# Kernel tuning notes

Hardware: AMD Instinct MI355X
Metric: run time of the kernel (lower is better)

## Reference

```python
import jax, jax.numpy as jnp
import numpy as np

D = 256      # embedding_dim
DI = 512     # inner dim = proj_factor * D
H = 4        # num heads
DH = DI // H # head dim
L = 4        # num blocks
K = 4        # causal conv kernel size

def _ln(x, g, b):
    mu = jnp.mean(x, -1, keepdims=True)
    v = jnp.var(x, -1, keepdims=True)
    return (x - mu) * jax.lax.rsqrt(v + 1e-5) * g + b

def _causal_conv(x, w, b):
    # x [B,S,DI], w [K,DI] depthwise causal conv
    S = x.shape[1]
    xp = jnp.pad(x, ((0, 0), (K - 1, 0), (0, 0)))
    out = b
    for j in range(K):
        out = out + xp[:, j:j + S, :] * w[j]
    return out

def _mlstm(q, k, v, ip, fp):
    # parallel stabilized mLSTM. q,k,v [B,S,H,DH]; ip,fp [B,S,H]
    q = q.transpose(0, 2, 1, 3)
    k = k.transpose(0, 2, 1, 3)
    v = v.transpose(0, 2, 1, 3)
    ip = ip.transpose(0, 2, 1)  # [B,H,S]
    fp = fp.transpose(0, 2, 1)
    lf = jax.nn.log_sigmoid(fp)                      # log forget gates
    Fc = jnp.cumsum(lf, axis=-1)
    Fc = jnp.concatenate([jnp.zeros_like(Fc[..., :1]), Fc], axis=-1)  # [B,H,S+1]
    logfg = Fc[..., 1:, None] - Fc[..., None, 1:]    # [B,H,S,S]: sum of log f over (s,t]
    S_len = q.shape[2]
    tri = jnp.tril(jnp.ones((S_len, S_len), dtype=bool))
    logD = jnp.where(tri, logfg + ip[..., None, :], jnp.float32(-1e30))
    m = jnp.max(logD, axis=-1, keepdims=True)        # stabilizer
    Dm = jnp.exp(logD - m)
    qk = jnp.einsum('bhtd,bhsd->bhts', q, k) * (DH ** -0.5)
    C = qk * Dm
    norm = jnp.maximum(jnp.abs(jnp.sum(C, axis=-1, keepdims=True)), jnp.exp(-m))
    h = jnp.einsum('bhts,bhsd->bhtd', C / (norm + 1e-6), v)
    return h.transpose(0, 2, 1, 3)

def _forward(x, time_features, Wp, bp, ln_g, ln_b, Wup, bup, conv_w, conv_b,
             Wq, Wk, Wv, Wif, bif, gn_g, gn_b, skip, Wdown, bdown,
             lnf_g, lnf_b, Wf, bf):
    B, S = x.shape
    xi = jnp.concatenate([x[..., None], time_features], axis=-1)  # [B,S,5]
    h = xi @ Wp + bp                                              # [B,S,D]
    for l in range(L):
        res = h
        hn = _ln(h, ln_g[l], ln_b[l])
        up = hn @ Wup[l] + bup[l]                 # [B,S,2*DI]
        xm, z = up[..., :DI], up[..., DI:]
        xc = jax.nn.silu(_causal_conv(xm, conv_w[l], conv_b[l]))
        q = (xc @ Wq[l]).reshape(B, S, H, DH)
        k = (xc @ Wk[l]).reshape(B, S, H, DH)
        v = (xm @ Wv[l]).reshape(B, S, H, DH)
        gi = jnp.concatenate([q.reshape(B, S, DI), k.reshape(B, S, DI), v.reshape(B, S, DI)], axis=-1)
        gates = gi @ Wif[l] + bif[l]              # [B,S,2H]
        ht = _mlstm(q, k, v, gates[..., :H], gates[..., H:])  # [B,S,H,DH]
        ht = _ln(ht, gn_g[l].reshape(H, DH), gn_b[l].reshape(H, DH)).reshape(B, S, DI)
        ht = ht + skip[l] * xc
        ht = ht * jax.nn.silu(z)
        h = res + ht @ Wdown[l] + bdown[l]
    h = _ln(h, lnf_g, lnf_b)
    return h[:, -1, :] @ Wf + bf                  # [B,1]

def setup_inputs():
    key = jax.random.key(0)
    ks = jax.random.split(key, 16)
    B, S = 8, 1024
    sd = jnp.float32(0.02)
    return {
        'x': jax.random.normal(ks[0], (B, S), jnp.float32),
        'time_features': jax.random.normal(ks[1], (B, S, 4), jnp.float32),
        'Wp': jax.random.normal(ks[2], (5, D)) * sd, 'bp': jnp.zeros((D,)),
        'ln_g': jnp.ones((L, D)), 'ln_b': jnp.zeros((L, D)),
        'Wup': jax.random.normal(ks[3], (L, D, 2 * DI)) * sd, 'bup': jnp.zeros((L, 2 * DI)),
        'conv_w': jax.random.normal(ks[4], (L, K, DI)) * sd, 'conv_b': jnp.zeros((L, DI)),
        'Wq': jax.random.normal(ks[5], (L, DI, DI)) * sd,
        'Wk': jax.random.normal(ks[6], (L, DI, DI)) * sd,
        'Wv': jax.random.normal(ks[7], (L, DI, DI)) * sd,
        'Wif': jax.random.normal(ks[8], (L, 3 * DI, 2 * H)) * sd, 'bif': jnp.zeros((L, 2 * H)),
        'gn_g': jnp.ones((L, DI)), 'gn_b': jnp.zeros((L, DI)),
        'skip': jnp.ones((L, DI)),
        'Wdown': jax.random.normal(ks[9], (L, DI, D)) * sd, 'bdown': jnp.zeros((L, D)),
        'lnf_g': jnp.ones((D,)), 'lnf_b': jnp.zeros((D,)),
        'Wf': jax.random.normal(ks[10], (D, 1)) * sd, 'bf': jnp.zeros((1,)),
    }

def reference(x, time_features, Wp, bp, ln_g, ln_b, Wup, bup, conv_w, conv_b,
              Wq, Wk, Wv, Wif, bif, gn_g, gn_b, skip, Wdown, bdown,
              lnf_g, lnf_b, Wf, bf):
    return _forward(x, time_features, Wp, bp, ln_g, ln_b, Wup, bup, conv_w, conv_b,
                    Wq, Wk, Wv, Wif, bif, gn_g, gn_b, skip, Wdown, bdown,
                    lnf_g, lnf_b, Wf, bf)
```

## Files before the change

### kernel.cpp

```cpp
#include <hip/hip_runtime.h>
#include <hip/hip_bf16.h>
#include <math.h>

#define S 1024
#define NLAYER 4

typedef __bf16 bf16x8 __attribute__((ext_vector_type(8)));
typedef float floatx4 __attribute__((ext_vector_type(4)));

__device__ __forceinline__ float wave_sum(float v) {
  #pragma unroll
  for (int off = 32; off > 0; off >>= 1) v += __shfl_xor(v, off, 64);
  return v;
}

__device__ __forceinline__ void wtrans_body(
    int bid, const float* Wup, const float* Wq, const float* Wk, const float* Wv,
    const float* Wdown, __bf16* WupT, __bf16* WqkT, __bf16* WvT, __bf16* WdownT) {
  __shared__ float T[32][33];
  int layer = bid / 1152, rr = bid % 1152;
  const float* src; __bf16* dst; int K, N, tile;
  if (rr < 256)       { src = Wup   + layer * 262144; dst = WupT  + layer * 262144;          K = 256; N = 1024; tile = rr; }
  else if (rr < 512)  { src = Wq    + layer * 262144; dst = WqkT  + layer * 524288;          K = 512; N = 512;  tile = rr - 256; }
  else if (rr < 768)  { src = Wk    + layer * 262144; dst = WqkT  + layer * 524288 + 262144; K = 512; N = 512;  tile = rr - 512; }
  else if (rr < 1024) { src = Wv    + layer * 262144; dst = WvT   + layer * 262144;          K = 512; N = 512;  tile = rr - 768; }
  else                { src = Wdown + layer * 131072; dst = WdownT + layer * 131072;         K = 512; N = 256;  tile = rr - 1024; }
  int ntn = N >> 5;
  int tk = tile / ntn, tn = tile % ntn;
  int tid = threadIdx.x;
  int r = tid >> 3, c4 = (tid & 7) * 4;
  float4 v = *(const float4*)(src + (size_t)(tk * 32 + r) * N + tn * 32 + c4);
  T[c4 + 0][r] = v.x; T[c4 + 1][r] = v.y; T[c4 + 2][r] = v.z; T[c4 + 3][r] = v.w;
  __syncthreads();
  __bf16 o[4];
  #pragma unroll
  for (int j = 0; j < 4; ++j) o[j] = (__bf16)T[r][c4 + j];
  *(uint2*)(dst + (size_t)(tn * 32 + r) * K + tk * 32 + c4) = *(uint2*)o;
}

__device__ __forceinline__ void wgprep_body(
    int bid, const float* Wq, const float* Wk, const float* Wv,
    const float* Wif, float* wg) {
  int l = bid >> 8;
  int rem = bid & 255;
  int sel = rem >> 7;
  int kg = rem & 127;
  int tid = threadIdx.x;
  int wv = tid >> 6, lane = tid & 63;
  int k = kg * 4 + wv;
  const float* wif = Wif + (size_t)l * 1536 * 8;
  float part[8] = {0, 0, 0, 0, 0, 0, 0, 0};
  if (sel == 0) {
    const float* qr = Wq + (size_t)l * 262144 + (size_t)k * 512;
    const float* kr = Wk + (size_t)l * 262144 + (size_t)k * 512;
    #pragma unroll
    for (int i = 0; i < 8; ++i) {
      int n = lane + i * 64;
      float qv = qr[n], kv = kr[n];
      const float* wq8 = wif + (size_t)n * 8;
      const float* wk8 = wif + (size_t)(512 + n) * 8;
      #pragma unroll
      for (int j = 0; j < 8; ++j) part[j] += qv * wq8[j] + kv * wk8[j];
    }
  } else {
    const float* vr = Wv + (size_t)l * 262144 + (size_t)k * 512;
    #pragma unroll
    for (int i = 0; i < 8; ++i) {
      int n = lane + i * 64;
      float vv = vr[n];
      const float* wv8 = wif + (size_t)(1024 + n) * 8;
      #pragma unroll
      for (int j = 0; j < 8; ++j) part[j] += vv * wv8[j];
    }
  }
  #pragma unroll
  for (int j = 0; j < 8; ++j) part[j] = wave_sum(part[j]);
  if (lane < 8) wg[(size_t)l * 8192 + sel * 4096 + (size_t)k * 8 + lane] = part[lane];
}

__device__ __forceinline__ void embed_body(
    int row, const float* x, const float* tf, const float* Wp, const float* bp,
    const float* g, const float* b, float* h, __bf16* hn) {
  int n = threadIdx.x;
  float xv = x[row];
  const float* t4 = tf + (size_t)row * 4;
  float acc = bp[n] + xv * Wp[n];
  acc += t4[0] * Wp[256 + n];
  acc += t4[1] * Wp[512 + n];
  acc += t4[2] * Wp[768 + n];
  acc += t4[3] * Wp[1024 + n];
  h[(size_t)row * 256 + n] = acc;
  __shared__ float red[4];
  int wid = n >> 6, lane = n & 63;
  float s = wave_sum(acc);
  if (lane == 0) red[wid] = s;
  __syncthreads();
  float mu = (red[0] + red[1] + red[2] + red[3]) * (1.f / 256.f);
  __syncthreads();
  float d = acc - mu;
  float s2 = wave_sum(d * d);
  if (lane == 0) red[wid] = s2;
  __syncthreads();
  float var = (red[0] + red[1] + red[2] + red[3]) * (1.f / 256.f);
  float rs = rsqrtf(var + 1e-5f);
  hn[(size_t)row * 256 + n] = (__bf16)(d * rs * g[n] + b[n]);
}

__global__ __launch_bounds__(256) void prep_kernel(
    const float* __restrict__ x, const float* __restrict__ tf,
    const float* __restrict__ Wp, const float* __restrict__ bp,
    const float* __restrict__ ln_g, const float* __restrict__ ln_b,
    const float* __restrict__ Wup, const float* __restrict__ Wq,
    const float* __restrict__ Wk, const float* __restrict__ Wv,
    const float* __restrict__ Wdown, const float* __restrict__ Wif,
    __bf16* __restrict__ WupT, __bf16* __restrict__ WqkT,
    __bf16* __restrict__ WvT, __bf16* __restrict__ WdownT,
    float* __restrict__ wg, float* __restrict__ h, __bf16* __restrict__ hn) {
  int bid = blockIdx.x;
  if (bid < 4608) {
    wtrans_body(bid, Wup, Wq, Wk, Wv, Wdown, WupT, WqkT, WvT, WdownT);
  } else if (bid < 4608 + 1024) {
    wgprep_body(bid - 4608, Wq, Wk, Wv, Wif, wg);
  } else {
    embed_body(bid - 5632, x, tf, Wp, bp, ln_g, ln_b, h, hn);
  }
}

__global__ __launch_bounds__(256) void ln256_kernel(
    const float* __restrict__ x, const float* __restrict__ g,
    const float* __restrict__ b, __bf16* __restrict__ y) {
  int row = blockIdx.x, tid = threadIdx.x;
  __shared__ float red[4];
  float v = x[(size_t)row * 256 + tid];
  float s = wave_sum(v);
  int wid = tid >> 6, lane = tid & 63;
  if (lane == 0) red[wid] = s;
  __syncthreads();
  float mu = (red[0] + red[1] + red[2] + red[3]) * (1.f / 256.f);
  __syncthreads();
  float d = v - mu;
  float s2 = wave_sum(d * d);
  if (lane == 0) red[wid] = s2;
  __syncthreads();
  float var = (red[0] + red[1] + red[2] + red[3]) * (1.f / 256.f);
  float rs = rsqrtf(var + 1e-5f);
  y[(size_t)row * 256 + tid] = (__bf16)(d * rs * g[tid] + b[tid]);
}

template <int TM, int MODE, int ACC>
__device__ __forceinline__ void hgemm_body(
    char* smem_raw,
    const __bf16* __restrict__ A, int lda,
    const __bf16* __restrict__ BT, int Kdim,
    const float* __restrict__ bias,
    void* __restrict__ Cout, int ldc, int bxi, int byi) {
  auto As = (__bf16(*)[40])smem_raw;
  auto Bs = (__bf16(*)[40])(smem_raw + (size_t)TM * 80);
  int tid = threadIdx.x;
  int bm = bxi * TM, bn = byi * 128;
  int wid = tid >> 6, lane = tid & 63;
  int wr = wid >> 1, wc = wid & 1;
  int lg = lane >> 4, li = lane & 15;
  constexpr int MI = TM / 32;
  constexpr int WROW = TM / 2;
  floatx4 acc[MI][4];
  #pragma unroll
  for (int i = 0; i < MI; ++i)
    #pragma unroll
    for (int j = 0; j < 4; ++j) acc[i][j] = (floatx4)(0.f);

  int arow = tid >> 2, aseg = tid & 3;
  bf16x8 pa0, pa1, pb0, pb1;
  auto pre = [&](int k0) {
    pa0 = *(const bf16x8*)(A + (size_t)(bm + arow) * lda + k0 + aseg * 8);
    if constexpr (TM == 128)
      pa1 = *(const bf16x8*)(A + (size_t)(bm + arow + 64) * lda + k0 + aseg * 8);
    pb0 = *(const bf16x8*)(BT + (size_t)(bn + arow) * Kdim + k0 + aseg * 8);
    pb1 = *(const bf16x8*)(BT + (size_t)(bn + arow + 64) * Kdim + k0 + aseg * 8);
  };
  pre(0);
  for (int k0 = 0; k0 < Kdim; k0 += 32) {
    __syncthreads();
    if constexpr (TM == 128) {
      *(bf16x8*)&As[arow][aseg * 8] = pa0;
      *(bf16x8*)&As[arow + 64][aseg * 8] = pa1;
    } else {
      *(bf16x8*)&As[arow][aseg * 8] = pa0;
    }
    *(bf16x8*)&Bs[arow][aseg * 8] = pb0;
    *(bf16x8*)&Bs[arow + 64][aseg * 8] = pb1;
    __syncthreads();
    if (k0 + 32 < Kdim) pre(k0 + 32);
    bf16x8 af[MI], bfr[4];
    #pragma unroll
    for (int mi = 0; mi < MI; ++mi)
      af[mi] = *(const bf16x8*)&As[wr * WROW + mi * 16 + li][lg * 8];
    #pragma unroll
    for (int ni = 0; ni < 4; ++ni)
      bfr[ni] = *(const bf16x8*)&Bs[wc * 64 + ni * 16 + li][lg * 8];
    #pragma unroll
    for (int mi = 0; mi < MI; ++mi)
      #pragma unroll
      for (int ni = 0; ni < 4; ++ni)
        acc[mi][ni] = __builtin_amdgcn_mfma_f32_16x16x32_bf16(af[mi], bfr[ni], acc[mi][ni], 0, 0, 0);
  }
  if constexpr (MODE == 1) {
    __bf16* eb = (__bf16*)smem_raw;
    const int PITCH = 136;
    __bf16* C = (__bf16*)Cout;
    #pragma unroll
    for (int mi = 0; mi < MI; ++mi) {
      __syncthreads();
      #pragma unroll
      for (int ni = 0; ni < 4; ++ni) {
        int col = wc * 64 + ni * 16 + li;
        float bz = bias ? bias[bn + col] : 0.f;
        #pragma unroll
        for (int r = 0; r < 4; ++r) {
          int lr = wr * 16 + lg * 4 + r;
          eb[lr * PITCH + col] = (__bf16)(acc[mi][ni][r] + bz);
        }
      }
      __syncthreads();
      #pragma unroll
      for (int i = 0; i < 2; ++i) {
        int lr = (tid >> 4) + i * 16;
        int c8 = (tid & 15) * 8;
        bf16x8 v = *(const bf16x8*)&eb[lr * PITCH + c8];
        int row_g = bm + (lr >> 4) * 64 + mi * 16 + (lr & 15);
        *(bf16x8*)(C + (size_t)row_g * ldc + bn + c8) = v;
      }
    }
  } else {
    #pragma unroll
    for (int mi = 0; mi < MI; ++mi) {
      int row = bm + wr * WROW + mi * 16 + lg * 4;
      #pragma unroll
      for (int ni = 0; ni < 4; ++ni) {
        int col = bn + wc * 64 + ni * 16 + li;
        if constexpr (MODE == 2) {
          __bf16 o4[4];
          #pragma unroll
          for (int r = 0; r < 4; ++r) o4[r] = (__bf16)acc[mi][ni][r];
          __bf16* vt = (__bf16*)Cout;
          size_t off = ((size_t)((row >> 10) * 4 + (col >> 7)) * 128 + (col & 127)) * 1024 + (row & 1023);
          *(uint2*)(vt + off) = *(uint2*)o4;
        } else {
          float bz = bias ? bias[col] : 0.f;
          float* C = (float*)Cout;
          #pragma unroll
          for (int r = 0; r < 4; ++r) {
            float v = acc[mi][ni][r] + bz;
            if (ACC) v += C[(size_t)(row + r) * ldc + col];
            C[(size_t)(row + r) * ldc + col] = v;
          }
        }
      }
    }
  }
}

template <int TM, int MODE, int ACC>
__global__ __launch_bounds__(256) void hgemm(
    const __bf16* __restrict__ A, int lda,
    const __bf16* __restrict__ BT, int Kdim,
    const float* __restrict__ bias,
    void* __restrict__ Cout, int ldc) {
  extern __shared__ char smem[];
  hgemm_body<TM, MODE, ACC>(smem, A, lda, BT, Kdim, bias, Cout, ldc,
                            blockIdx.x, blockIdx.y);
}

__global__ __launch_bounds__(256) void qkv_kernel(
    const __bf16* __restrict__ xc, const __bf16* __restrict__ WqkT,
    __bf16* __restrict__ qk, const __bf16* __restrict__ up,
    const __bf16* __restrict__ WvT, __bf16* __restrict__ vT) {
  extern __shared__ char smem[];
  if (blockIdx.y < 8) {
    hgemm_body<128, 1, 0>(smem, xc, 512, WqkT, 512, nullptr, qk, 1024,
                          blockIdx.x, blockIdx.y);
  } else {
    int j = blockIdx.y - 8;
    hgemm_body<64, 2, 0>(smem, up, 1024, WvT, 512, nullptr, vT, 0,
                         blockIdx.x * 2 + (j & 1), j >> 1);
  }
}

__global__ __launch_bounds__(256) void conv_silu_kernel(
    const __bf16* __restrict__ up, const float* __restrict__ cw,
    const float* __restrict__ cb, const float* __restrict__ wg,
    const float* __restrict__ bif, __bf16* __restrict__ xc,
    float* __restrict__ gates) {
  int tid = threadIdx.x;
  int wv = tid >> 6, lane = tid & 63;
  int row = blockIdx.x * 4 + wv;
  int c8 = lane * 8;
  int t = row & (S - 1);
  float acc[8];
  *(float4*)&acc[0] = *(const float4*)(cb + c8);
  *(float4*)&acc[4] = *(const float4*)(cb + c8 + 4);
  float xm[8];
  #pragma unroll
  for (int j = 0; j < 4; ++j) {
    int tt = t - 3 + j;
    if (tt >= 0) {
      bf16x8 xv = *(const bf16x8*)(up + (size_t)(row - 3 + j) * 1024 + c8);
      float4 w0 = *(const float4*)(cw + j * 512 + c8);
      float4 w1 = *(const float4*)(cw + j * 512 + c8 + 4);
      acc[0] += w0.x * (float)xv[0]; acc[1] += w0.y * (float)xv[1];
      acc[2] += w0.z * (float)xv[2]; acc[3] += w0.w * (float)xv[3];
      acc[4] += w1.x * (float)xv[4]; acc[5] += w1.y * (float)xv[5];
      acc[6] += w1.z * (float)xv[6]; acc[7] += w1.w * (float)xv[7];
      if (j == 3) {
        #pragma unroll
        for (int m = 0; m < 8; ++m) xm[m] = (float)xv[m];
      }
    }
  }
  bf16x8 o;
  float xcs[8];
  #pragma unroll
  for (int m = 0; m < 8; ++m) {
    float sg = 1.f / (1.f + __expf(-acc[m]));
    xcs[m] = acc[m] * sg;
    o[m] = (__bf16)xcs[m];
  }
  *(bf16x8*)(xc + (size_t)row * 512 + c8) = o;
  const float* w1 = wg + (size_t)c8 * 8;
  const float* w2 = wg + 4096 + (size_t)c8 * 8;
  float part[8] = {0, 0, 0, 0, 0, 0, 0, 0};
  #pragma unroll
  for (int m = 0; m < 8; ++m) {
    const float* a = w1 + m * 8;
    const float* b = w2 + m * 8;
    #pragma unroll
    for (int j = 0; j < 8; ++j) part[j] += xcs[m] * a[j] + xm[m] * b[j];
  }
  #pragma unroll
  for (int j = 0; j < 8; ++j) part[j] = wave_sum(part[j]);
  if (lane < 8) gates[(size_t)row * 8 + lane] = part[lane] + bif[lane];
}

__global__ __launch_bounds__(64) void scan_kernel(
    const float* __restrict__ gates, float* __restrict__ gout,
    float* __restrict__ Mout, float* __restrict__ NFout) {
  int bh = blockIdx.x;
  int bb = bh >> 2, hh = bh & 3;
  int lane = threadIdx.x;
  float ip[16], pf[16];
  #pragma unroll
  for (int i = 0; i < 16; ++i) {
    int t = lane * 16 + i;
    const float* grow = gates + ((size_t)(bb * S + t)) * 8;
    ip[i] = grow[hh];
    float fp = grow[4 + hh];
    float lf = fminf(fp, 0.f) - log1pf(__expf(-fabsf(fp)));
    pf[i] = (i == 0) ? lf : pf[i - 1] + lf;
  }
  float T = pf[15];
  float inc = T;
  #pragma unroll
  for (int off = 1; off < 64; off <<= 1) {
    float v = __shfl_up(inc, off, 64);
    if (lane >= off) inc += v;
  }
  float excl = inc - T;
  float F[16], g[16], pm[16];
  #pragma unroll
  for (int i = 0; i < 16; ++i) {
    F[i] = excl + pf[i];
    g[i] = ip[i] - F[i];
    pm[i] = (i == 0) ? g[0] : fmaxf(pm[i - 1], g[i]);
  }
  float Mx = pm[15];
  float incm = Mx;
  #pragma unroll
  for (int off = 1; off < 64; off <<= 1) {
    float v = __shfl_up(incm, off, 64);
    if (lane >= off) incm = fmaxf(incm, v);
  }
  float em = __shfl_up(incm, 1, 64);
  if (lane == 0) em = -3.4e38f;
  #pragma unroll
  for (int i = 0; i < 16; ++i) {
    int t = lane * 16 + i;
    size_t o = (size_t)bh * S + t;
    float M = fmaxf(em, pm[i]);
    gout[o] = g[i];
    Mout[o] = M;
    NFout[o] = __expf(-F[i] - M);
  }
}

__global__ __launch_bounds__(256, 1) void attn_kernel(
    const __bf16* __restrict__ qk, const __bf16* __restrict__ vT,
    const float* __restrict__ gbuf, const float* __restrict__ Mbuf,
    const float* __restrict__ NFbuf,
    const float* __restrict__ gn_g, const float* __restrict__ gn_b,
    const float* __restrict__ skip,
    const __bf16* __restrict__ xc, const __bf16* __restrict__ up,
    __bf16* __restrict__ hd) {
  __shared__ __bf16 Ks[64][136];
  __shared__ __bf16 Vs[128][72];
  __shared__ __bf16 plds[4][2][16][72];
  __shared__ float gls[64];
  __shared__ float glds[128], blds[128], slds[128];
  int px = blockIdx.y, bh = blockIdx.x;
  int tqA = px, tqB = 15 - px;
  int bb = bh >> 2, hh = bh & 3;
  int tid = threadIdx.x;
  int wv = tid >> 6, lane = tid & 63;
  int lg = lane >> 4, li = lane & 15;
  int tbA = tqA * 64 + wv * 16;
  int tbB = tqB * 64 + wv * 16;
  const float scale = 0.08838834764831845f;

  if (tid < 128) {
    glds[tid] = gn_g[hh * 128 + tid];
    blds[tid] = gn_b[hh * 128 + tid];
    slds[tid] = skip[hh * 128 + tid];
  }

  bf16x8 aqA[4], aqB[4];
  {
    const __bf16* qpA = qk + ((size_t)(bb * S + tbA + li)) * 1024 + hh * 128 + lg * 8;
    const __bf16* qpB = qk + ((size_t)(bb * S + tbB + li)) * 1024 + hh * 128 + lg * 8;
    #pragma unroll
    for (int cd = 0; cd < 4; ++cd) {
      aqA[cd] = *(const bf16x8*)(qpA + cd * 32);
      aqB[cd] = *(const bf16x8*)(qpB + cd * 32);
    }
  }
  float mlA[4], nfA[4], mlB[4], nfB[4];
  #pragma unroll
  for (int r = 0; r < 4; ++r) {
    mlA[r] = Mbuf[(size_t)bh * S + tbA + lg * 4 + r];
    nfA[r] = NFbuf[(size_t)bh * S + tbA + lg * 4 + r];
    mlB[r] = Mbuf[(size_t)bh * S + tbB + lg * 4 + r];
    nfB[r] = NFbuf[(size_t)bh * S + tbB + lg * 4 + r];
  }

  floatx4 oA[8], oB[8];
  #pragma unroll
  for (int df = 0; df < 8; ++df) { oA[df] = (floatx4)(0.f); oB[df] = (floatx4)(0.f); }
  float rsA[4] = {0, 0, 0, 0}, rsB[4] = {0, 0, 0, 0};

  int krow = tid >> 3, kcol = tid & 7;
  bf16x8 kreg[4], vreg[4];
  float greg = 0.f;
  auto preload = [&](int st) {
    int s0 = st * 64;
    const __bf16* kp = qk + ((size_t)(bb * S + s0 + krow)) * 1024 + 512 + hh * 128;
    kreg[0] = *(const bf16x8*)(kp + kcol * 8);
    kreg[1] = *(const bf16x8*)(kp + (size_t)32 * 1024 + kcol * 8);
    kreg[2] = *(const bf16x8*)(kp + 64 + kcol * 8);
    kreg[3] = *(const bf16x8*)(kp + (size_t)32 * 1024 + 64 + kcol * 8);
    #pragma unroll
    for (int i = 0; i < 4; ++i)
      vreg[i] = *(const bf16x8*)(vT + ((size_t)(bh * 128 + krow + i * 32)) * 1024 + s0 + kcol * 8);
    if (tid < 64) greg = gbuf[(size_t)bh * S + s0 + tid];
  };
  preload(0);

  for (int st = 0; st <= tqB; ++st) {
    __syncthreads();
    *(bf16x8*)&Ks[krow][kcol * 8] = kreg[0];
    *(bf16x8*)&Ks[krow + 32][kcol * 8] = kreg[1];
    *(bf16x8*)&Ks[krow][64 + kcol * 8] = kreg[2];
    *(bf16x8*)&Ks[krow + 32][64 + kcol * 8] = kreg[3];
    #pragma unroll
    for (int i = 0; i < 4; ++i) *(bf16x8*)&Vs[krow + i * 32][kcol * 8] = vreg[i];
    if (tid < 64) gls[tid] = greg;
    __syncthreads();
    if (st < tqB) preload(st + 1);

    int s0 = st * 64;
    bool actA = (st <= tqA);
    #pragma unroll
    for (int ns = 0; ns < 4; ++ns) {
      bf16x8 bk0 = *(const bf16x8*)&Ks[ns * 16 + li][lg * 8];
      bf16x8 bk1 = *(const bf16x8*)&Ks[ns * 16 + li][32 + lg * 8];
      bf16x8 bk2 = *(const bf16x8*)&Ks[ns * 16 + li][64 + lg * 8];
      bf16x8 bk3 = *(const bf16x8*)&Ks[ns * 16 + li][96 + lg * 8];
      int s = s0 + ns * 16 + li;
      float gv = gls[ns * 16 + li];
      if (actA) {
        floatx4 pa = (floatx4)(0.f);
        pa = __builtin_amdgcn_mfma_f32_16x16x32_bf16(aqA[0], bk0, pa, 0, 0, 0);
        pa = __builtin_amdgcn_mfma_f32_16x16x32_bf16(aqA[1], bk1, pa, 0, 0, 0);
        pa = __builtin_amdgcn_mfma_f32_16x16x32_bf16(aqA[2], bk2, pa, 0, 0, 0);
        pa = __builtin_amdgcn_mfma_f32_16x16x32_bf16(aqA[3], bk3, pa, 0, 0, 0);
        #pragma unroll
        for (int r = 0; r < 4; ++r) {
          int t = tbA + lg * 4 + r;
          float val = pa[r] * scale * __expf(gv - mlA[r]);
          float w = (s <= t) ? val : 0.f;
          rsA[r] += w;
          plds[wv][0][lg * 4 + r][ns * 16 + li] = (__bf16)w;
        }
      }
      {
        floatx4 pb = (floatx4)(0.f);
        pb = __builtin_amdgcn_mfma_f32_16x16x32_bf16(aqB[0], bk0, pb, 0, 0, 0);
        pb = __builtin_amdgcn_mfma_f32_16x16x32_bf16(aqB[1], bk1, pb, 0, 0, 0);
        pb = __builtin_amdgcn_mfma_f32_16x16x32_bf16(aqB[2], bk2, pb, 0, 0, 0);
        pb = __builtin_amdgcn_mfma_f32_16x16x32_bf16(aqB[3], bk3, pb, 0, 0, 0);
        #pragma unroll
        for (int r = 0; r < 4; ++r) {
          int t = tbB + lg * 4 + r;
          float val = pb[r] * scale * __expf(gv - mlB[r]);
          float w = (s <= t) ? val : 0.f;
          rsB[r] += w;
          plds[wv][1][lg * 4 + r][ns * 16 + li] = (__bf16)w;
        }
      }
    }
    bf16x8 apA0, apA1, apB0, apB1;
    if (actA) {
      apA0 = *(const bf16x8*)&plds[wv][0][li][lg * 8];
      apA1 = *(const bf16x8*)&plds[wv][0][li][32 + lg * 8];
    }
    apB0 = *(const bf16x8*)&plds[wv][1][li][lg * 8];
    apB1 = *(const bf16x8*)&plds[wv][1][li][32 + lg * 8];
    #pragma unroll
    for (int df = 0; df < 8; ++df) {
      bf16x8 bv0 = *(const bf16x8*)&Vs[df * 16 + li][lg * 8];
      bf16x8 bv1 = *(const bf16x8*)&Vs[df * 16 + li][32 + lg * 8];
      if (actA) {
        oA[df] = __builtin_amdgcn_mfma_f32_16x16x32_bf16(apA0, bv0, oA[df], 0, 0, 0);
        oA[df] = __builtin_amdgcn_mfma_f32_16x16x32_bf16(apA1, bv1, oA[df], 0, 0, 0);
      }
      oB[df] = __builtin_amdgcn_mfma_f32_16x16x32_bf16(apB0, bv0, oB[df], 0, 0, 0);
      oB[df] = __builtin_amdgcn_mfma_f32_16x16x32_bf16(apB1, bv1, oB[df], 0, 0, 0);
    }
  }
  #pragma unroll
  for (int r = 0; r < 4; ++r) {
    float a = rsA[r], b = rsB[r];
    a += __shfl_xor(a, 1, 64); a += __shfl_xor(a, 2, 64);
    a += __shfl_xor(a, 4, 64); a += __shfl_xor(a, 8, 64);
    b += __shfl_xor(b, 1, 64); b += __shfl_xor(b, 2, 64);
    b += __shfl_xor(b, 4, 64); b += __shfl_xor(b, 8, 64);
    rsA[r] = a; rsB[r] = b;
  }
  #pragma unroll
  for (int tile = 0; tile < 2; ++tile) {
    int tb = tile == 0 ? tbA : tbB;
    #pragma unroll
    for (int r = 0; r < 4; ++r) {
      float rs = tile == 0 ? rsA[r] : rsB[r];
      float nf = tile == 0 ? nfA[r] : nfB[r];
      float inv = 1.f / (fmaxf(fabsf(rs), nf) + 1e-6f);
      float v8[8], s1 = 0.f, s2 = 0.f;
      #pragma unroll
      for (int df = 0; df < 8; ++df) {
        float v = (tile == 0 ? oA[df][r] : oB[df][r]) * inv;
        v8[df] = v;
        s1 += v;
        s2 += v * v;
      }
      s1 += __shfl_xor(s1, 1, 64); s1 += __shfl_xor(s1, 2, 64);
      s1 += __shfl_xor(s1, 4, 64); s1 += __shfl_xor(s1, 8, 64);
      s2 += __shfl_xor(s2, 1, 64); s2 += __shfl_xor(s2, 2, 64);
      s2 += __shfl_xor(s2, 4, 64); s2 += __shfl_xor(s2, 8, 64);
      float mu = s1 * (1.f / 128.f);
      float var = s2 * (1.f / 128.f) - mu * mu;
      float rq = rsqrtf(var + 1e-5f);
      int t = tb + lg * 4 + r;
      const __bf16* xr = xc + ((size_t)(bb * S + t)) * 512 + hh * 128 + li;
      const __bf16* zr = up + ((size_t)(bb * S + t)) * 1024 + 512 + hh * 128 + li;
      __bf16* od = hd + ((size_t)(bb * S + t)) * 512 + hh * 128 + li;
      #pragma unroll
      for (int df = 0; df < 8; ++df) {
        int c = df * 16 + li;
        float ln = (v8[df] - mu) * rq * glds[c] + blds[c];
        float val = ln + slds[c] * (float)xr[df * 16];
        float z = (float)zr[df * 16];
        float sg = 1.f / (1.f + __expf(-z));
        od[df * 16] = (__bf16)(val * (z * sg));
      }
    }
  }
}

__global__ __launch_bounds__(256) void final_kernel(
    const float* __restrict__ h, const float* __restrict__ g,
    const float* __restrict__ b, const float* __restrict__ Wf,
    const float* __restrict__ bf, float* __restrict__ out) {
  int bb = blockIdx.x, tid = threadIdx.x;
  size_t row = (size_t)(bb * S + S - 1) * 256;
  __shared__ float red[4];
  float v = h[row + tid];
  float s = wave_sum(v);
  int wid = tid >> 6, lane = tid & 63;
  if (lane == 0) red[wid] = s;
  __syncthreads();
  float mu = (red[0] + red[1] + red[2] + red[3]) * (1.f / 256.f);
  __syncthreads();
  float d = v - mu;
  float s2 = wave_sum(d * d);
  if (lane == 0) red[wid] = s2;
  __syncthreads();
  float var = (red[0] + red[1] + red[2] + red[3]) * (1.f / 256.f);
  float rs = rsqrtf(var + 1e-5f);
  float ln = d * rs * g[tid] + b[tid];
  float p = ln * Wf[tid];
  float psum = wave_sum(p);
  __syncthreads();
  if (lane == 0) red[wid] = psum;
  __syncthreads();
  if (tid == 0) out[bb] = red[0] + red[1] + red[2] + red[3] + bf[0];
}

extern "C" void kernel_launch(void* const* d_in, const int* in_sizes, int n_in,
                              void* d_out, int out_size, void* d_ws, size_t ws_size,
                              hipStream_t stream) {
  const float* x      = (const float*)d_in[0];
  const float* tf     = (const float*)d_in[1];
  const float* Wp     = (const float*)d_in[2];
  const float* bp     = (const float*)d_in[3];
  const float* ln_g   = (const float*)d_in[4];
  const float* ln_b   = (const float*)d_in[5];
  const float* Wup    = (const float*)d_in[6];
  const float* bup    = (const float*)d_in[7];
  const float* conv_w = (const float*)d_in[8];
  const float* conv_b = (const float*)d_in[9];
  const float* Wq     = (const float*)d_in[10];
  const float* Wk     = (const float*)d_in[11];
  const float* Wv     = (const float*)d_in[12];
  const float* Wif    = (const float*)d_in[13];
  const float* bif    = (const float*)d_in[14];
  const float* gn_g   = (const float*)d_in[15];
  const float* gn_b   = (const float*)d_in[16];
  const float* skip   = (const float*)d_in[17];
  const float* Wdown  = (const float*)d_in[18];
  const float* bdown  = (const float*)d_in[19];
  const float* lnf_g  = (const float*)d_in[20];
  const float* lnf_b  = (const float*)d_in[21];
  const float* Wf     = (const float*)d_in[22];
  const float* bf     = (const float*)d_in[23];
  float* out = (float*)d_out;

  float* h     = (float*)d_ws;
  float* gates = h + 2097152;
  float* gbuf  = gates + 65536;
  float* Mbuf  = gbuf + 32768;
  float* NFbuf = Mbuf + 32768;
  float* wgbuf = NFbuf + 32768;
  __bf16* hn   = (__bf16*)(wgbuf + 32768);
  __bf16* up   = hn + 2097152;
  __bf16* xc   = up + 8388608;
  __bf16* qk   = xc + 4194304;
  __bf16* vT   = qk + 8388608;
  __bf16* hd   = vT + 4194304;
  __bf16* WupT   = hd + 4194304;
  __bf16* WqkT   = WupT + 1048576;
  __bf16* WvT    = WqkT + 2097152;
  __bf16* WdownT = WvT + 1048576;

  prep_kernel<<<13824, 256, 0, stream>>>(
      x, tf, Wp, bp, ln_g, ln_b, Wup, Wq, Wk, Wv, Wdown, Wif,
      WupT, WqkT, WvT, WdownT, wgbuf, h, hn);
  for (int l = 0; l < NLAYER; ++l) {
    if (l > 0)
      ln256_kernel<<<8192, 256, 0, stream>>>(h, ln_g + l * 256, ln_b + l * 256, hn);
    hgemm<128, 1, 0><<<dim3(64, 8), 256, 20480, stream>>>(
        hn, 256, WupT + (size_t)l * 262144, 256, bup + l * 1024, up, 1024);
    conv_silu_kernel<<<2048, 256, 0, stream>>>(up, conv_w + l * 2048, conv_b + l * 512,
                                               wgbuf + l * 8192, bif + l * 8, xc, gates);
    scan_kernel<<<32, 64, 0, stream>>>(gates, gbuf, Mbuf, NFbuf);
    qkv_kernel<<<dim3(64, 16), 256, 20480, stream>>>(
        xc, WqkT + (size_t)l * 524288, qk, up, WvT + (size_t)l * 262144, vT);
    attn_kernel<<<dim3(32, 8), 256, 0, stream>>>(
        qk, vT, gbuf, Mbuf, NFbuf, gn_g + l * 512, gn_b + l * 512, skip + l * 512,
        xc, up, hd);
    hgemm<64, 0, 1><<<dim3(128, 2), 256, 15360, stream>>>(
        hd, 512, WdownT + (size_t)l * 131072, 512, bdown + l * 256, h, 256);
  }
  final_kernel<<<8, 256, 0, stream>>>(h, lnf_g, lnf_b, Wf, bf, out);
}
```

Before: 674.1 us.

## Fuse down-projection GEMM with residual add and next-layer LayerNorm

Replaces the down-projection hgemm and the separate ln256 kernel with one kernel whose blocks own full 256-wide rows (32 rows each). The epilogue adds bias and residual, writes h, and computes row mean and variance through shuffles and shared memory to emit the next layer's bf16 LN output. This removes one launch per layer and a re-read of h. In exchange it uses only 256 blocks, each loading the entire 256-column weight slice, and computes variance as E[x²]-mu², which is less numerically stable.

```diff
diff --git a/kernel.cpp b/kernel.cpp
--- a/kernel.cpp
+++ b/kernel.cpp
@@ -126,27 +126,6 @@
   }
 }
 
-__global__ __launch_bounds__(256) void ln256_kernel(
-    const float* __restrict__ x, const float* __restrict__ g,
-    const float* __restrict__ b, __bf16* __restrict__ y) {
-  int row = blockIdx.x, tid = threadIdx.x;
-  __shared__ float red[4];
-  float v = x[(size_t)row * 256 + tid];
-  float s = wave_sum(v);
-  int wid = tid >> 6, lane = tid & 63;
-  if (lane == 0) red[wid] = s;
-  __syncthreads();
-  float mu = (red[0] + red[1] + red[2] + red[3]) * (1.f / 256.f);
-  __syncthreads();
-  float d = v - mu;
-  float s2 = wave_sum(d * d);
-  if (lane == 0) red[wid] = s2;
-  __syncthreads();
-  float var = (red[0] + red[1] + red[2] + red[3]) * (1.f / 256.f);
-  float rs = rsqrtf(var + 1e-5f);
-  y[(size_t)row * 256 + tid] = (__bf16)(d * rs * g[tid] + b[tid]);
-}
-
 template <int TM, int MODE, int ACC>
 __device__ __forceinline__ void hgemm_body(
     char* smem_raw,
@@ -181,12 +160,8 @@
   pre(0);
   for (int k0 = 0; k0 < Kdim; k0 += 32) {
     __syncthreads();
-    if constexpr (TM == 128) {
-      *(bf16x8*)&As[arow][aseg * 8] = pa0;
-      *(bf16x8*)&As[arow + 64][aseg * 8] = pa1;
-    } else {
-      *(bf16x8*)&As[arow][aseg * 8] = pa0;
-    }
+    *(bf16x8*)&As[arow][aseg * 8] = pa0;
+    if constexpr (TM == 128) *(bf16x8*)&As[arow + 64][aseg * 8] = pa1;
     *(bf16x8*)&Bs[arow][aseg * 8] = pb0;
     *(bf16x8*)&Bs[arow + 64][aseg * 8] = pb1;
     __syncthreads();
@@ -283,6 +258,86 @@
     int j = blockIdx.y - 8;
     hgemm_body<64, 2, 0>(smem, up, 1024, WvT, 512, nullptr, vT, 0,
                          blockIdx.x * 2 + (j & 1), j >> 1);
+  }
+}
+
+__global__ __launch_bounds__(256) void dgemm_ln_kernel(
+    const __bf16* __restrict__ A, const __bf16* __restrict__ BT,
+    const float* __restrict__ bias, float* __restrict__ h,
+    const float* __restrict__ lng, const float* __restrict__ lnb,
+    __bf16* __restrict__ hn) {
+  __shared__ __bf16 As[32][40];
+  __shared__ __bf16 Bs[256][40];
+  __shared__ float redS[2][32], redQ[2][32];
+  int tid = threadIdx.x;
+  int bm = blockIdx.x * 32;
+  int wid = tid >> 6, lane = tid & 63;
+  int wr = wid >> 1, wc = wid & 1;
+  int lg = lane >> 4, li = lane & 15;
+  floatx4 acc[8];
+  #pragma unroll
+  for (int j = 0; j < 8; ++j) acc[j] = (floatx4)(0.f);
+
+  int arow = tid >> 2, aseg = tid & 3;
+  bf16x8 pa, pb[4];
+  auto pre = [&](int k0) {
+    if (tid < 128)
+      pa = *(const bf16x8*)(A + (size_t)(bm + arow) * 512 + k0 + aseg * 8);
+    #pragma unroll
+    for (int i = 0; i < 4; ++i)
+      pb[i] = *(const bf16x8*)(BT + (size_t)(arow + i * 64) * 512 + k0 + aseg * 8);
+  };
+  pre(0);
+  for (int k0 = 0; k0 < 512; k0 += 32) {
+    __syncthreads();
+    if (tid < 128) *(bf16x8*)&As[arow][aseg * 8] = pa;
+    #pragma unroll
+    for (int i = 0; i < 4; ++i) *(bf16x8*)&Bs[arow + i * 64][aseg * 8] = pb[i];
+    __syncthreads();
+    if (k0 + 32 < 512) pre(k0 + 32);
+    bf16x8 af = *(const bf16x8*)&As[wr * 16 + li][lg * 8];
+    #pragma unroll
+    for (int ni = 0; ni < 8; ++ni) {
+      bf16x8 bfr = *(const bf16x8*)&Bs[wc * 128 + ni * 16 + li][lg * 8];
+      acc[ni] = __builtin_amdgcn_mfma_f32_16x16x32_bf16(af, bfr, acc[ni], 0, 0, 0);
+    }
+  }
+  #pragma unroll
+  for (int r = 0; r < 4; ++r) {
+    int lr = wr * 16 + lg * 4 + r;
+    int row = bm + lr;
+    float s1 = 0.f, s2 = 0.f;
+    #pragma unroll
+    for (int ni = 0; ni < 8; ++ni) {
+      int col = wc * 128 + ni * 16 + li;
+      float v = acc[ni][r] + bias[col] + h[(size_t)row * 256 + col];
+      acc[ni][r] = v;
+      h[(size_t)row * 256 + col] = v;
+      s1 += v;
+      s2 += v * v;
+    }
+    s1 += __shfl_xor(s1, 1, 64); s1 += __shfl_xor(s1, 2, 64);
+    s1 += __shfl_xor(s1, 4, 64); s1 += __shfl_xor(s1, 8, 64);
+    s2 += __shfl_xor(s2, 1, 64); s2 += __shfl_xor(s2, 2, 64);
+    s2 += __shfl_xor(s2, 4, 64); s2 += __shfl_xor(s2, 8, 64);
+    if (li == 0) { redS[wc][lr] = s1; redQ[wc][lr] = s2; }
+  }
+  if (!lng) return;
+  __syncthreads();
+  #pragma unroll
+  for (int r = 0; r < 4; ++r) {
+    int lr = wr * 16 + lg * 4 + r;
+    int row = bm + lr;
+    float s1 = redS[0][lr] + redS[1][lr];
+    float s2 = redQ[0][lr] + redQ[1][lr];
+    float mu = s1 * (1.f / 256.f);
+    float var = s2 * (1.f / 256.f) - mu * mu;
+    float rs = rsqrtf(var + 1e-5f);
+    #pragma unroll
+    for (int ni = 0; ni < 8; ++ni) {
+      int col = wc * 128 + ni * 16 + li;
+      hn[(size_t)row * 256 + col] = (__bf16)((acc[ni][r] - mu) * rs * lng[col] + lnb[col]);
+    }
   }
 }
 
@@ -662,8 +717,6 @@
       x, tf, Wp, bp, ln_g, ln_b, Wup, Wq, Wk, Wv, Wdown, Wif,
       WupT, WqkT, WvT, WdownT, wgbuf, h, hn);
   for (int l = 0; l < NLAYER; ++l) {
-    if (l > 0)
-      ln256_kernel<<<8192, 256, 0, stream>>>(h, ln_g + l * 256, ln_b + l * 256, hn);
     hgemm<128, 1, 0><<<dim3(64, 8), 256, 20480, stream>>>(
         hn, 256, WupT + (size_t)l * 262144, 256, bup + l * 1024, up, 1024);
     conv_silu_kernel<<<2048, 256, 0, stream>>>(up, conv_w + l * 2048, conv_b + l * 512,
@@ -674,8 +727,10 @@
     attn_kernel<<<dim3(32, 8), 256, 0, stream>>>(
         qk, vT, gbuf, Mbuf, NFbuf, gn_g + l * 512, gn_b + l * 512, skip + l * 512,
         xc, up, hd);
-    hgemm<64, 0, 1><<<dim3(128, 2), 256, 15360, stream>>>(
-        hd, 512, WdownT + (size_t)l * 131072, 512, bdown + l * 256, h, 256);
+    const float* lng = (l + 1 < NLAYER) ? (ln_g + (l + 1) * 256) : nullptr;
+    const float* lnb = (l + 1 < NLAYER) ? (ln_b + (l + 1) * 256) : nullptr;
+    dgemm_ln_kernel<<<256, 256, 0, stream>>>(
+        hd, WdownT + (size_t)l * 131072, bdown + l * 256, h, lng, lnb, hn);
   }
   final_kernel<<<8, 256, 0, stream>>>(h, lnf_g, lnf_b, Wf, bf, out);
 }
```

Result: faster. 641.9 us (-4.8%).
